# Kernel optimization log

Measured on AMD Instinct MI355X. Metric: run time of the kernel, lower is better.

Reference implementation:

```python
import jax, jax.numpy as jnp
import numpy as np

N_NODES = 100000
N_EDGES = 3200000
IN_CH, HID, OUT = 128, 32, 2
LN_EPS = 1e-5


def _layer_norm(x, g, b):
    mu = jnp.mean(x, axis=-1, keepdims=True)
    var = jnp.mean((x - mu) ** 2, axis=-1, keepdims=True)
    return (x - mu) * jax.lax.rsqrt(var + LN_EPS) * g + b


def _gcn_conv(x, W, b, src, dst, dinv_sqrt, dinv, n):
    # PyG GCNConv with add_self_loops=True: out = D^-1/2 (A+I) D^-1/2 (x W) + b
    xw = x @ W                                           # [N, F_out]
    coeff = (dinv_sqrt[src] * dinv_sqrt[dst])[:, None]    # [E, 1]
    agg = jax.ops.segment_sum(xw[src] * coeff, dst, num_segments=n)
    # self-loop contribution: norm = d^-1/2 * d^-1/2 = 1/d
    return agg + xw * dinv[:, None] + b


def setup_inputs() -> dict:
    key = jax.random.key(0)
    ks = jax.random.split(key, 12)
    x = jax.random.normal(ks[0], (N_NODES, IN_CH), jnp.float32)
    edge_index = jax.random.randint(ks[1], (2, N_EDGES), 0, N_NODES)

    def glorot(k, fi, fo):
        return jax.random.normal(k, (fi, fo), jnp.float32) * np.float32(1.0 / np.sqrt(fi))

    return {
        "x": x,
        "edge_index": edge_index,
        "W1": glorot(ks[2], IN_CH, HID), "b1": jnp.zeros((HID,), jnp.float32),
        "g1": jnp.ones((HID,), jnp.float32), "be1": jnp.zeros((HID,), jnp.float32),
        "W2": glorot(ks[3], HID, HID), "b2": jnp.zeros((HID,), jnp.float32),
        "g2": jnp.ones((HID,), jnp.float32), "be2": jnp.zeros((HID,), jnp.float32),
        "W3": glorot(ks[4], HID, OUT), "b3": jnp.zeros((OUT,), jnp.float32),
    }


def reference(x, edge_index, W1, b1, g1, be1, W2, b2, g2, be2, W3, b3):
    n = x.shape[0]
    src, dst = edge_index[0], edge_index[1]
    # degree with self-loops (unit edge weights)
    deg = jax.ops.segment_sum(jnp.ones(src.shape[0], x.dtype), dst, num_segments=n) + 1.0
    dinv_sqrt = jax.lax.rsqrt(deg)
    dinv = 1.0 / deg

    h = _gcn_conv(x, W1, b1, src, dst, dinv_sqrt, dinv, n)
    h = jax.nn.relu(_layer_norm(h, g1, be1))  # dropout is identity in eval mode
    h = _gcn_conv(h, W2, b2, src, dst, dinv_sqrt, dinv, n)
    h = jax.nn.relu(_layer_norm(h, g2, be2))
    logits = _gcn_conv(h, W3, b3, src, dst, dinv_sqrt, dinv, n)
    return logits
```

## Files before the change

kernel.cpp:

```cpp
#include <hip/hip_runtime.h>

#define NN 100000
#define NE 3200000
#define NB 391
#define CAP 9216
#define CHUNK 6250
#define NSBLK 512
#define LN_EPS 1e-5f

__device__ __forceinline__ unsigned short f2bf(float f) {
  unsigned b = __float_as_uint(f);
  b += 0x7FFF + ((b >> 16) & 1);
  return (unsigned short)(b >> 16);
}


__global__ __launch_bounds__(256) void k_init(int* __restrict__ bcur) {
  int i = blockIdx.x * 256 + threadIdx.x;
  if (i < NB) bcur[i] = i * CAP;
}


__global__ __launch_bounds__(256) void k_bucket(const int* __restrict__ src, const int* __restrict__ dst,
                                                int* __restrict__ bcur, unsigned* __restrict__ packed) {
  __shared__ int lh[NB];
  __shared__ int lstart[NB];
  __shared__ int lg[NB];
  __shared__ int sc[512];
  __shared__ unsigned buf[CHUNK];
  int tid = threadIdx.x;
  for (int i = tid; i < NB; i += 256) lh[i] = 0;
  __syncthreads();
  int base = blockIdx.x * CHUNK;
  int dreg[25], sreg[25];
  #pragma unroll
  for (int k = 0; k < 25; ++k) {
    int idx = tid + k * 256;
    int e = base + idx;
    bool v = (idx < CHUNK) && (e < NE);
    dreg[k] = v ? dst[e] : -1;
    sreg[k] = v ? src[e] : 0;
    if (v) atomicAdd(&lh[dreg[k] >> 8], 1);
  }
  __syncthreads();
  int ia = tid, ib = tid + 256;
  sc[ia] = (ia < NB) ? lh[ia] : 0;
  sc[ib] = (ib < NB) ? lh[ib] : 0;
  __syncthreads();
  for (int off = 1; off < 512; off <<= 1) {
    int va = (ia >= off) ? sc[ia - off] : 0;
    int vb = (ib >= off) ? sc[ib - off] : 0;
    __syncthreads();
    sc[ia] += va;
    sc[ib] += vb;
    __syncthreads();
  }
  if (ia < NB) lstart[ia] = sc[ia] - lh[ia];
  if (ib < NB) lstart[ib] = sc[ib] - lh[ib];
  for (int i = tid; i < NB; i += 256) {
    int c = lh[i];
    lg[i] = c ? atomicAdd(&bcur[i], c) : 0;
  }
  __syncthreads();
  for (int i = tid; i < NB; i += 256) lh[i] = 0;
  __syncthreads();
  #pragma unroll
  for (int k = 0; k < 25; ++k) {
    int d = dreg[k];
    if (d >= 0) {
      int b = d >> 8;
      int r = atomicAdd(&lh[b], 1);
      buf[lstart[b] + r] = (unsigned)sreg[k] | ((unsigned)(d & 255) << 24);
    }
  }
  __syncthreads();
  int hw = tid >> 5, l = tid & 31;
  for (int b = hw; b < NB; b += 8) {
    int cnt = lh[b], st = lstart[b], gp = lg[b];
    for (int j = l; j < cnt; j += 32) packed[gp + j] = buf[st + j];
  }
}


__global__ __launch_bounds__(256) void k_nodesort(const unsigned* __restrict__ packed,
                                                  const int* __restrict__ bcur,
                                                  int* __restrict__ csr, int* __restrict__ noff,
                                                  int* __restrict__ ncnt, float* __restrict__ ds) {
  __shared__ int h[256], lstart[256], cur[256], sc[256];
  int tid = threadIdx.x;
  h[tid] = 0;
  __syncthreads();
  int b = blockIdx.x;
  int o = b * CAP, e1 = bcur[b];
  for (int i = o + tid; i < e1; i += 256) atomicAdd(&h[packed[i] >> 24], 1);
  __syncthreads();
  int c = h[tid];
  sc[tid] = c;
  __syncthreads();
  for (int off = 1; off < 256; off <<= 1) {
    int v = (tid >= off) ? sc[tid - off] : 0;
    __syncthreads();
    sc[tid] += v;
    __syncthreads();
  }
  int ex = sc[tid] - c;
  lstart[tid] = ex;
  cur[tid] = 0;
  int n = b * 256 + tid;
  if (n < NN) {
    noff[n] = o + ex;
    ncnt[n] = c;
    ds[n] = rsqrtf((float)c + 1.0f);
  }
  __syncthreads();
  for (int i = o + tid; i < e1; i += 256) {
    unsigned e = packed[i];
    int dl = e >> 24;
    int r = atomicAdd(&cur[dl], 1);
    csr[o + lstart[dl] + r] = (int)(e & 0xFFFFFF);
  }
}


__global__ __launch_bounds__(256) void k_gemm1(const float* __restrict__ x, const float* __restrict__ W1,
                                               const float* __restrict__ ds,
                                               unsigned short* __restrict__ xw1h) {
  __shared__ float Wt[32][132];
  __shared__ float xr[8][128];
  for (int idx = threadIdx.x; idx < 4096; idx += 256) {
    int k = idx >> 5, c = idx & 31;
    Wt[c][k] = W1[idx];
  }
  __syncthreads();
  int g = threadIdx.x >> 5, lane = threadIdx.x & 31;
  for (int tile = blockIdx.x; tile < NN / 8; tile += gridDim.x) {
    int row = tile * 8 + g;
    float4 xv = *(const float4*)&x[row * 128 + lane * 4];
    *(float4*)&xr[g][lane * 4] = xv;
    __builtin_amdgcn_wave_barrier();
    float acc = 0.f;
    #pragma unroll
    for (int k4 = 0; k4 < 32; ++k4) {
      float4 a = *(const float4*)&xr[g][k4 * 4];
      float4 b = *(const float4*)&Wt[lane][k4 * 4];
      acc = fmaf(a.x, b.x, acc);
      acc = fmaf(a.y, b.y, acc);
      acc = fmaf(a.z, b.z, acc);
      acc = fmaf(a.w, b.w, acc);
    }
    xw1h[row * 32 + lane] = f2bf(acc * ds[row]);
    __builtin_amdgcn_wave_barrier();
  }
}


template <int NOUT>
__global__ __launch_bounds__(256, 4) void k_csragg(const unsigned* __restrict__ xwsh, const int* __restrict__ csr,
    const int* __restrict__ noff, const int* __restrict__ ncnt, const float* __restrict__ ds,
    const float* __restrict__ bias, const float* __restrict__ gam, const float* __restrict__ bet,
    const float* __restrict__ Wn, void* __restrict__ outp) {
  __shared__ float Wl[1024];
  int tid = threadIdx.x;
  if (NOUT == 32) {
    for (int i = tid; i < 1024; i += 256) Wl[i] = Wn[i];
    __syncthreads();
  }
  int g = tid >> 4, l = tid & 15;
  int n = blockIdx.x * 16 + g;
  int o = noff[n], end = o + ncnt[n];
  float2 a0 = {0.f, 0.f}, a1 = {0.f, 0.f}, a2 = {0.f, 0.f}, a3 = {0.f, 0.f};
  int i = o;
  for (; i + 16 <= end; i += 16) {
    int s[16];
    #pragma unroll
    for (int k = 0; k < 16; ++k) s[k] = csr[i + k];
    unsigned u[16];
    #pragma unroll
    for (int k = 0; k < 16; ++k) u[k] = xwsh[s[k] * 16 + l];
    #pragma unroll
    for (int k = 0; k < 16; ++k) {
      float vx = __uint_as_float(u[k] << 16);
      float vy = __uint_as_float(u[k] & 0xFFFF0000u);
      if ((k & 3) == 0)      { a0.x += vx; a0.y += vy; }
      else if ((k & 3) == 1) { a1.x += vx; a1.y += vy; }
      else if ((k & 3) == 2) { a2.x += vx; a2.y += vy; }
      else                   { a3.x += vx; a3.y += vy; }
    }
  }
  for (; i + 4 <= end; i += 4) {
    int s[4];
    #pragma unroll
    for (int k = 0; k < 4; ++k) s[k] = csr[i + k];
    unsigned u[4];
    #pragma unroll
    for (int k = 0; k < 4; ++k) u[k] = xwsh[s[k] * 16 + l];
    a0.x += __uint_as_float(u[0] << 16); a0.y += __uint_as_float(u[0] & 0xFFFF0000u);
    a1.x += __uint_as_float(u[1] << 16); a1.y += __uint_as_float(u[1] & 0xFFFF0000u);
    a2.x += __uint_as_float(u[2] << 16); a2.y += __uint_as_float(u[2] & 0xFFFF0000u);
    a3.x += __uint_as_float(u[3] << 16); a3.y += __uint_as_float(u[3] & 0xFFFF0000u);
  }
  for (; i < end; ++i) {
    unsigned u = xwsh[csr[i] * 16 + l];
    a0.x += __uint_as_float(u << 16); a0.y += __uint_as_float(u & 0xFFFF0000u);
  }
  float dsn = ds[n];
  unsigned us = xwsh[n * 16 + l];
  float2 bi = ((const float2*)bias)[l];
  float2 val;
  val.x = dsn * ((a0.x + a1.x) + (a2.x + a3.x) + __uint_as_float(us << 16)) + bi.x;
  val.y = dsn * ((a0.y + a1.y) + (a2.y + a3.y) + __uint_as_float(us & 0xFFFF0000u)) + bi.y;
  float part = val.x + val.y;
  #pragma unroll
  for (int o2 = 8; o2 > 0; o2 >>= 1) part += __shfl_xor(part, o2, 16);
  float mu = part * (1.f / 32.f);
  float2 d = {val.x - mu, val.y - mu};
  float sq = d.x * d.x + d.y * d.y;
  #pragma unroll
  for (int o2 = 8; o2 > 0; o2 >>= 1) sq += __shfl_xor(sq, o2, 16);
  float rs = rsqrtf(sq * (1.f / 32.f) + LN_EPS);
  float2 ga = ((const float2*)gam)[l];
  float2 be = ((const float2*)bet)[l];
  float2 h;
  h.x = fmaxf(d.x * rs * ga.x + be.x, 0.f);
  h.y = fmaxf(d.y * rs * ga.y + be.y, 0.f);
  if (NOUT == 32) {
    float2 acc = {0.f, 0.f};
    #pragma unroll
    for (int c2 = 0; c2 < 16; ++c2) {
      float hx = __shfl(h.x, c2, 16);
      float hy = __shfl(h.y, c2, 16);
      float2 w0 = *(const float2*)&Wl[(2 * c2) * 32 + 2 * l];
      float2 w1 = *(const float2*)&Wl[(2 * c2 + 1) * 32 + 2 * l];
      acc.x = fmaf(hx, w0.x, acc.x); acc.y = fmaf(hx, w0.y, acc.y);
      acc.x = fmaf(hy, w1.x, acc.x); acc.y = fmaf(hy, w1.y, acc.y);
    }
    ((unsigned*)outp)[n * 16 + l] =
        (unsigned)f2bf(acc.x * dsn) | ((unsigned)f2bf(acc.y * dsn) << 16);
  } else {
    float4 wv = ((const float4*)Wn)[l];
    float p0 = h.x * wv.x + h.y * wv.z;
    float p1 = h.x * wv.y + h.y * wv.w;
    #pragma unroll
    for (int o2 = 8; o2 > 0; o2 >>= 1) { p0 += __shfl_xor(p0, o2, 16); p1 += __shfl_xor(p1, o2, 16); }
    if (l == 0) {
      float2 r = {p0 * dsn, p1 * dsn};
      *(float2*)&((float*)outp)[n * 2] = r;
    }
  }
}


__global__ __launch_bounds__(256) void k_fin2(const float* __restrict__ xws, const int* __restrict__ csr,
    const int* __restrict__ noff, const int* __restrict__ ncnt, const float* __restrict__ ds,
    const float* __restrict__ b3, float* __restrict__ out) {
  int tid = threadIdx.x;
  int hw = tid >> 5, l = tid & 31;
  int n = blockIdx.x * 8 + hw;
  int o = noff[n], end = o + ncnt[n];
  float a0 = 0.f, a1 = 0.f;
  for (int i = o + l; i < end; i += 32) {
    int s = csr[i];
    float2 v = *(const float2*)&xws[s * 2];
    a0 += v.x; a1 += v.y;
  }
  for (int o2 = 16; o2 > 0; o2 >>= 1) { a0 += __shfl_xor(a0, o2, 32); a1 += __shfl_xor(a1, o2, 32); }
  if (l == 0) {
    float dsn = ds[n];
    float2 sv = *(const float2*)&xws[n * 2];
    out[n * 2]     = dsn * (a0 + sv.x) + b3[0];
    out[n * 2 + 1] = dsn * (a1 + sv.y) + b3[1];
  }
}

extern "C" void kernel_launch(void* const* d_in, const int* in_sizes, int n_in,
                              void* d_out, int out_size, void* d_ws, size_t ws_size,
                              hipStream_t stream) {
  (void)in_sizes; (void)n_in; (void)out_size; (void)ws_size;
  const float* x   = (const float*)d_in[0];
  const int*   ei  = (const int*)d_in[1];
  const float* W1  = (const float*)d_in[2];
  const float* b1  = (const float*)d_in[3];
  const float* g1  = (const float*)d_in[4];
  const float* be1 = (const float*)d_in[5];
  const float* W2  = (const float*)d_in[6];
  const float* b2  = (const float*)d_in[7];
  const float* g2  = (const float*)d_in[8];
  const float* be2 = (const float*)d_in[9];
  const float* W3  = (const float*)d_in[10];
  const float* b3  = (const float*)d_in[11];
  const int* src = ei;
  const int* dst = ei + NE;
  float* out = (float*)d_out;

  char* w = (char*)d_ws;
  int*      bcur   = (int*)(w);
  int*      noff   = (int*)(w + (64u << 10));
  int*      ncnt   = (int*)(w + (512u << 10));
  float*    ds     = (float*)(w + (1024u << 10));
  unsigned* packed = (unsigned*)(w + (2u << 20));
  int*      csr    = (int*)(w + (17u << 20));
  unsigned short* xw1h = (unsigned short*)(w + (2u << 20));
  float*    xw3s   = (float*)(w + (10u << 20));
  unsigned short* xw2h = (unsigned short*)(w + (32u << 20));

  k_init    <<<2,     256, 0, stream>>>(bcur);
  k_bucket  <<<NSBLK, 256, 0, stream>>>(src, dst, bcur, packed);
  k_nodesort<<<NB,    256, 0, stream>>>(packed, bcur, csr, noff, ncnt, ds);
  k_gemm1   <<<2048,  256, 0, stream>>>(x, W1, ds, xw1h);
  k_csragg<32><<<NN/16, 256, 0, stream>>>((const unsigned*)xw1h, csr, noff, ncnt, ds, b1, g1, be1, W2, xw2h);
  k_csragg<2> <<<NN/16, 256, 0, stream>>>((const unsigned*)xw2h, csr, noff, ncnt, ds, b2, g2, be2, W3, xw3s);
  k_fin2    <<<NN/8,  256, 0, stream>>>(xw3s, csr, noff, ncnt, ds, b3, out);
}
```

Measured before the change: 302.6 us.

## Trim bucket registers, use wave-shuffle scan in nodesort, re-pad gemm1 LDS

k_bucket stops holding src values in registers and instead re-reads src from global memory during the scatter pass, lowering register pressure. k_nodesort now launches 512 threads per block and replaces the 256-entry LDS Hillis-Steele scan with a per-wave shuffle scan plus a small cross-wave combine, which removes many barriers. k_gemm1 changes the W transpose padding from 132 to 130 and reads LDS with float2 instead of float4, aiming to cut bank conflicts. The csragg edits only add bf16 unpack helpers. The extra global read of src in k_bucket adds memory traffic in exchange for the register savings.

```diff
diff --git a/kernel.cpp b/kernel.cpp
--- a/kernel.cpp
+++ b/kernel.cpp
@@ -13,6 +13,8 @@
   b += 0x7FFF + ((b >> 16) & 1);
   return (unsigned short)(b >> 16);
 }
+__device__ __forceinline__ float bflo(unsigned u) { return __uint_as_float(u << 16); }
+__device__ __forceinline__ float bfhi(unsigned u) { return __uint_as_float(u & 0xFFFF0000u); }
 
 
 __global__ __launch_bounds__(256) void k_init(int* __restrict__ bcur) {
@@ -32,14 +34,13 @@
   for (int i = tid; i < NB; i += 256) lh[i] = 0;
   __syncthreads();
   int base = blockIdx.x * CHUNK;
-  int dreg[25], sreg[25];
+  int dreg[25];
   #pragma unroll
   for (int k = 0; k < 25; ++k) {
     int idx = tid + k * 256;
     int e = base + idx;
     bool v = (idx < CHUNK) && (e < NE);
     dreg[k] = v ? dst[e] : -1;
-    sreg[k] = v ? src[e] : 0;
     if (v) atomicAdd(&lh[dreg[k] >> 8], 1);
   }
   __syncthreads();
@@ -68,9 +69,10 @@
   for (int k = 0; k < 25; ++k) {
     int d = dreg[k];
     if (d >= 0) {
+      int e = base + tid + k * 256;
       int b = d >> 8;
       int r = atomicAdd(&lh[b], 1);
-      buf[lstart[b] + r] = (unsigned)sreg[k] | ((unsigned)(d & 255) << 24);
+      buf[lstart[b] + r] = (unsigned)src[e] | ((unsigned)(d & 255) << 24);
     }
   }
   __syncthreads();
@@ -82,38 +84,48 @@
 }
 
 
-__global__ __launch_bounds__(256) void k_nodesort(const unsigned* __restrict__ packed,
+__global__ __launch_bounds__(512) void k_nodesort(const unsigned* __restrict__ packed,
                                                   const int* __restrict__ bcur,
                                                   int* __restrict__ csr, int* __restrict__ noff,
                                                   int* __restrict__ ncnt, float* __restrict__ ds) {
-  __shared__ int h[256], lstart[256], cur[256], sc[256];
+  __shared__ int h[256], lstart[256], cur[256];
+  __shared__ int ws[4];
   int tid = threadIdx.x;
-  h[tid] = 0;
+  if (tid < 256) h[tid] = 0;
   __syncthreads();
   int b = blockIdx.x;
   int o = b * CAP, e1 = bcur[b];
-  for (int i = o + tid; i < e1; i += 256) atomicAdd(&h[packed[i] >> 24], 1);
-  __syncthreads();
-  int c = h[tid];
-  sc[tid] = c;
-  __syncthreads();
-  for (int off = 1; off < 256; off <<= 1) {
-    int v = (tid >= off) ? sc[tid - off] : 0;
-    __syncthreads();
-    sc[tid] += v;
-    __syncthreads();
-  }
-  int ex = sc[tid] - c;
-  lstart[tid] = ex;
-  cur[tid] = 0;
-  int n = b * 256 + tid;
-  if (n < NN) {
-    noff[n] = o + ex;
-    ncnt[n] = c;
-    ds[n] = rsqrtf((float)c + 1.0f);
-  }
-  __syncthreads();
-  for (int i = o + tid; i < e1; i += 256) {
+  for (int i = o + tid; i < e1; i += 512) atomicAdd(&h[packed[i] >> 24], 1);
+  __syncthreads();
+  int lane = tid & 63, w = tid >> 6;
+  int c = 0, x = 0;
+  if (tid < 256) {
+    c = h[tid];
+    x = c;
+    #pragma unroll
+    for (int off = 1; off < 64; off <<= 1) {
+      int t = __shfl_up(x, off);
+      if (lane >= off) x += t;
+    }
+    if (lane == 63) ws[w] = x;
+  }
+  __syncthreads();
+  if (tid < 256) {
+    int base2 = 0;
+    #pragma unroll
+    for (int j = 0; j < 3; ++j) if (j < w) base2 += ws[j];
+    int ex = base2 + x - c;
+    lstart[tid] = ex;
+    cur[tid] = 0;
+    int n = b * 256 + tid;
+    if (n < NN) {
+      noff[n] = o + ex;
+      ncnt[n] = c;
+      ds[n] = rsqrtf((float)c + 1.0f);
+    }
+  }
+  __syncthreads();
+  for (int i = o + tid; i < e1; i += 512) {
     unsigned e = packed[i];
     int dl = e >> 24;
     int r = atomicAdd(&cur[dl], 1);
@@ -125,7 +137,7 @@
 __global__ __launch_bounds__(256) void k_gemm1(const float* __restrict__ x, const float* __restrict__ W1,
                                                const float* __restrict__ ds,
                                                unsigned short* __restrict__ xw1h) {
-  __shared__ float Wt[32][132];
+  __shared__ float Wt[32][130];
   __shared__ float xr[8][128];
   for (int idx = threadIdx.x; idx < 4096; idx += 256) {
     int k = idx >> 5, c = idx & 31;
@@ -140,13 +152,11 @@
     __builtin_amdgcn_wave_barrier();
     float acc = 0.f;
     #pragma unroll
-    for (int k4 = 0; k4 < 32; ++k4) {
-      float4 a = *(const float4*)&xr[g][k4 * 4];
-      float4 b = *(const float4*)&Wt[lane][k4 * 4];
+    for (int k2 = 0; k2 < 64; ++k2) {
+      float2 a = *(const float2*)&xr[g][k2 * 2];
+      float2 b = *(const float2*)&Wt[lane][k2 * 2];
       acc = fmaf(a.x, b.x, acc);
       acc = fmaf(a.y, b.y, acc);
-      acc = fmaf(a.z, b.z, acc);
-      acc = fmaf(a.w, b.w, acc);
     }
     xw1h[row * 32 + lane] = f2bf(acc * ds[row]);
     __builtin_amdgcn_wave_barrier();
@@ -179,8 +189,7 @@
     for (int k = 0; k < 16; ++k) u[k] = xwsh[s[k] * 16 + l];
     #pragma unroll
     for (int k = 0; k < 16; ++k) {
-      float vx = __uint_as_float(u[k] << 16);
-      float vy = __uint_as_float(u[k] & 0xFFFF0000u);
+      float vx = bflo(u[k]), vy = bfhi(u[k]);
       if ((k & 3) == 0)      { a0.x += vx; a0.y += vy; }
       else if ((k & 3) == 1) { a1.x += vx; a1.y += vy; }
       else if ((k & 3) == 2) { a2.x += vx; a2.y += vy; }
@@ -194,21 +203,21 @@
     unsigned u[4];
     #pragma unroll
     for (int k = 0; k < 4; ++k) u[k] = xwsh[s[k] * 16 + l];
-    a0.x += __uint_as_float(u[0] << 16); a0.y += __uint_as_float(u[0] & 0xFFFF0000u);
-    a1.x += __uint_as_float(u[1] << 16); a1.y += __uint_as_float(u[1] & 0xFFFF0000u);
-    a2.x += __uint_as_float(u[2] << 16); a2.y += __uint_as_float(u[2] & 0xFFFF0000u);
-    a3.x += __uint_as_float(u[3] << 16); a3.y += __uint_as_float(u[3] & 0xFFFF0000u);
+    a0.x += bflo(u[0]); a0.y += bfhi(u[0]);
+    a1.x += bflo(u[1]); a1.y += bfhi(u[1]);
+    a2.x += bflo(u[2]); a2.y += bfhi(u[2]);
+    a3.x += bflo(u[3]); a3.y += bfhi(u[3]);
   }
   for (; i < end; ++i) {
     unsigned u = xwsh[csr[i] * 16 + l];
-    a0.x += __uint_as_float(u << 16); a0.y += __uint_as_float(u & 0xFFFF0000u);
+    a0.x += bflo(u); a0.y += bfhi(u);
   }
   float dsn = ds[n];
   unsigned us = xwsh[n * 16 + l];
   float2 bi = ((const float2*)bias)[l];
   float2 val;
-  val.x = dsn * ((a0.x + a1.x) + (a2.x + a3.x) + __uint_as_float(us << 16)) + bi.x;
-  val.y = dsn * ((a0.y + a1.y) + (a2.y + a3.y) + __uint_as_float(us & 0xFFFF0000u)) + bi.y;
+  val.x = dsn * ((a0.x + a1.x) + (a2.x + a3.x) + bflo(us)) + bi.x;
+  val.y = dsn * ((a0.y + a1.y) + (a2.y + a3.y) + bfhi(us)) + bi.y;
   float part = val.x + val.y;
   #pragma unroll
   for (int o2 = 8; o2 > 0; o2 >>= 1) part += __shfl_xor(part, o2, 16);
@@ -305,7 +314,7 @@
 
   k_init    <<<2,     256, 0, stream>>>(bcur);
   k_bucket  <<<NSBLK, 256, 0, stream>>>(src, dst, bcur, packed);
-  k_nodesort<<<NB,    256, 0, stream>>>(packed, bcur, csr, noff, ncnt, ds);
+  k_nodesort<<<NB,    512, 0, stream>>>(packed, bcur, csr, noff, ncnt, ds);
   k_gemm1   <<<2048,  256, 0, stream>>>(x, W1, ds, xw1h);
   k_csragg<32><<<NN/16, 256, 0, stream>>>((const unsigned*)xw1h, csr, noff, ncnt, ds, b1, g1, be1, W2, xw2h);
   k_csragg<2> <<<NN/16, 256, 0, stream>>>((const unsigned*)xw2h, csr, noff, ncnt, ds, b2, g2, be2, W3, xw3s);
```

New measurement: 313.6 us. +3.6%, slower.
